# Kernel tuning notes

Hardware: AMD Instinct MI355X
Metric: run time of the kernel (lower is better)

## Reference

```python
import jax, jax.numpy as jnp
import numpy as np

DIM = 128
L = 4
EPS = 1e-5


def setup_inputs() -> dict:
    key = jax.random.key(0)
    ks = jax.random.split(key, 16)
    g, n_per = 4096, 32
    n = g * n_per
    e = 4 * n
    s = 0.05
    inp = {
        "x_atoms": jax.random.randint(ks[0], (n, 2), 0, 3),
        "edge_index": jax.random.randint(ks[1], (2, e), 0, n),
        "edge_attr": jax.random.randint(ks[2], (e, 2), 0, 3),
        "batch": jnp.repeat(jnp.arange(g), n_per),
        "num_graphs": g,
        "max_nodes": n_per,
        "task_embs": jax.random.normal(ks[3], (g, DIM), jnp.float32),
        "teb": jax.random.normal(ks[4], (g, DIM), jnp.float32),
        "emb1": jax.random.normal(ks[5], (120, DIM), jnp.float32) * s,
        "emb2": jax.random.normal(ks[6], (3, DIM), jnp.float32) * s,
        "edge_e1": jax.random.normal(ks[7], (L, 6, DIM), jnp.float32) * s,
        "edge_e2": jax.random.normal(ks[8], (L, 3, DIM), jnp.float32) * s,
        "W1": jax.random.normal(ks[9], (L, DIM, 2 * DIM), jnp.float32) * s,
        "b1": jnp.zeros((L, 2 * DIM), jnp.float32),
        "W2": jax.random.normal(ks[10], (L, 2 * DIM, DIM), jnp.float32) * s,
        "b2": jnp.zeros((L, DIM), jnp.float32),
        "bn_w": jnp.ones((L, DIM), jnp.float32),
        "bn_b": jnp.zeros((L, DIM), jnp.float32),
        "film_Wg": jax.random.normal(ks[11], (2, DIM, DIM), jnp.float32) * s,
        "film_bg": jnp.zeros((2, DIM), jnp.float32),
        "film_Wb": jax.random.normal(ks[12], (2, DIM, DIM), jnp.float32) * s,
        "film_bb": jnp.zeros((2, DIM), jnp.float32),
    }
    return inp


def _gin_layer(x, src, dst, eattr, e1, e2, W1, b1, W2, b2):
    # GINConv (pretrain-gnns): scatter-add of (x_j + edge_emb) + self-loop (attr [4,0]), then 2-layer MLP.
    n = x.shape[0]
    emb = e1[eattr[:, 0]] + e2[eattr[:, 1]]                       # [E, D]
    agg = jax.ops.segment_sum(x[src] + emb, dst, num_segments=n)  # [N, D]
    agg = agg + x + (e1[4] + e2[0])                               # self loops
    h = jax.nn.relu(agg @ W1 + b1)
    return h @ W2 + b2


def _batchnorm(x, w, b):
    mu = jnp.mean(x, axis=0)
    var = jnp.var(x, axis=0)
    return (x - mu) * jax.lax.rsqrt(var + EPS) * w + b


def reference(x_atoms, edge_index, edge_attr, batch, num_graphs, max_nodes,
              task_embs, teb, emb1, emb2, edge_e1, edge_e2,
              W1, b1, W2, b2, bn_w, bn_b,
              film_Wg, film_bg, film_Wb, film_bb):
    g = int(num_graphs)
    n = x_atoms.shape[0]
    x = emb1[x_atoms[:, 0]] + emb2[x_atoms[:, 1]]                 # [N, D]
    # --- add virtual nodes (one per graph) and bidirectional virtual edges ---
    x = jnp.concatenate([x, teb], axis=0)                         # [N+g, D]
    dst0 = jnp.arange(n)
    vsrc = n + batch                                              # virtual node index per real node
    src_all = jnp.concatenate([edge_index[0], vsrc, dst0])
    dst_all = jnp.concatenate([edge_index[1], dst0, vsrc])
    v_attr = jnp.tile(jnp.array([[5, 0]], dtype=edge_attr.dtype), (2 * n, 1))
    eattr = jnp.concatenate([edge_attr, v_attr], axis=0)
    # --- positions within graph for to_dense_batch (batch is sorted) ---
    counts = jnp.bincount(batch, length=g)
    offsets = jnp.cumsum(counts) - counts
    pos = dst0 - offsets[batch]
    for layer in range(L):
        x = _gin_layer(x, src_all, dst_all, eattr,
                       edge_e1[layer], edge_e2[layer],
                       W1[layer], b1[layer], W2[layer], b2[layer])
        if layer in (1, 3):
            xv = x[n:]
            dense = jnp.zeros((g, int(max_nodes), DIM), x.dtype).at[batch, pos].set(x[:n])
            fl = layer // 3
            gamma = task_embs @ film_Wg[fl] + film_bg[fl]          # [g, D]
            beta = task_embs @ film_Wb[fl] + film_bb[fl]
            dense = gamma[:, None, :] * dense + beta[:, None, :]
            x = jnp.concatenate([dense[batch, pos], xv], axis=0)   # masked_select inverse
        x = _batchnorm(x, bn_w[layer], bn_b[layer])
        if layer != L - 1:
            x = jax.nn.relu(x)
        # dropout is identity in eval mode
    return x[:n]
```

## Files before the change

### kernel.cpp

```cpp
#include <hip/hip_runtime.h>
#include <hip/hip_bf16.h>

typedef __bf16 bf16_t;
typedef bf16_t bf16x8 __attribute__((ext_vector_type(8)));
typedef float f32x4 __attribute__((ext_vector_type(4)));

#define EPSV 1e-5f

__global__ void k_zerof(float* p, int cnt) {
  int i = blockIdx.x * 256 + threadIdx.x;
  if (i < cnt) p[i] = 0.f;
}
__global__ void k_zeroi(int* p, int cnt) {
  int i = blockIdx.x * 256 + threadIdx.x;
  if (i < cnt) p[i] = 0;
}

__global__ void k_prep_weights(const float* __restrict__ W1, const float* __restrict__ W2,
                               bf16_t* __restrict__ W1T, bf16_t* __restrict__ W2T, int total) {
  int idx = blockIdx.x * 256 + threadIdx.x;
  if (idx >= total) return;
  int l = idx >> 15, r = idx & 32767;
  int k = r >> 8, c = r & 255;
  W1T[(l << 15) + c * 128 + k] = (bf16_t)W1[idx];
  int k2 = r >> 7, c2 = r & 127;
  W2T[(l << 15) + c2 * 256 + k2] = (bf16_t)W2[idx];
}

__global__ void k_prep_film(const float* __restrict__ Wg, const float* __restrict__ Wb,
                            bf16_t* __restrict__ fWT) {
  int idx = blockIdx.x * 256 + threadIdx.x;
  if (idx >= 4 * 16384) return;
  int m = idx >> 14, r = idx & 16383;
  int c = r >> 7, k = r & 127;
  const float* W = ((m & 1) ? Wb : Wg) + (m >> 1) * 16384;
  fWT[idx] = (bf16_t)W[k * 128 + c];
}

__global__ void k_prep_te(const float* __restrict__ te, bf16_t* __restrict__ teb_out, int total) {
  int idx = blockIdx.x * 256 + threadIdx.x;
  if (idx < total) teb_out[idx] = (bf16_t)te[idx];
}

__global__ void k_ecomb(const float* __restrict__ e1, const float* __restrict__ e2,
                        float* __restrict__ ec, int total) {
  int idx = blockIdx.x * 256 + threadIdx.x;
  if (idx >= total) return;
  int ch = idx & 127;
  int t = idx >> 7;
  int comb = t % 18, l = t / 18;
  int i = comb / 3, j = comb % 3;
  ec[idx] = e1[(l * 6 + i) * 128 + ch] + e2[(l * 3 + j) * 128 + ch];
}

__launch_bounds__(256, 2)
__global__ void k_film(const bf16_t* __restrict__ teb, const bf16_t* __restrict__ fWT,
                       const float* __restrict__ bg, const float* __restrict__ bb,
                       float* __restrict__ gbuf, int g) {
  const int mat = blockIdx.x & 3;
  const int r0 = (blockIdx.x >> 2) * 64;
  const int tid = threadIdx.x;
  const int wave = tid >> 6, lane = tid & 63;
  const int lr = lane & 15, lk = lane >> 4;
  const int w32 = wave * 32;
  const bf16_t* W = fWT + mat * 16384;
  const float* B = ((mat & 1) ? bb : bg) + (mat >> 1) * 128;

  bf16x8 bbf[2][4];
  #pragma unroll
  for (int cf = 0; cf < 2; ++cf)
    #pragma unroll
    for (int kk = 0; kk < 4; ++kk)
      bbf[cf][kk] = *(const bf16x8*)(W + ((w32 + cf * 16 + lr) << 7) + kk * 32 + (lk << 3));

  f32x4 acc[4][2];
  f32x4 zero4 = {0.f, 0.f, 0.f, 0.f};
  #pragma unroll
  for (int rf = 0; rf < 4; ++rf)
    #pragma unroll
    for (int cf = 0; cf < 2; ++cf) acc[rf][cf] = zero4;

  #pragma unroll
  for (int kk = 0; kk < 4; ++kk) {
    bf16x8 a[4];
    #pragma unroll
    for (int rf = 0; rf < 4; ++rf)
      a[rf] = *(const bf16x8*)(teb + ((size_t)(r0 + rf * 16 + lr) << 7) + kk * 32 + (lk << 3));
    #pragma unroll
    for (int rf = 0; rf < 4; ++rf)
      #pragma unroll
      for (int cf = 0; cf < 2; ++cf)
        acc[rf][cf] = __builtin_amdgcn_mfma_f32_16x16x32_bf16(a[rf], bbf[cf][kk], acc[rf][cf], 0, 0, 0);
  }

  float* out = gbuf + (size_t)mat * g * 128;
  #pragma unroll
  for (int cf = 0; cf < 2; ++cf) {
    int col = w32 + cf * 16 + lr;
    float bias = B[col];
    #pragma unroll
    for (int rf = 0; rf < 4; ++rf)
      #pragma unroll
      for (int j = 0; j < 4; ++j) {
        int row = r0 + rf * 16 + lk * 4 + j;
        out[(size_t)row * 128 + col] = acc[rf][cf][j] + bias;
      }
  }
}

__global__ void k_init_x(const int* __restrict__ xa, const float* __restrict__ teb,
                         const float* __restrict__ emb1, const float* __restrict__ emb2,
                         bf16_t* __restrict__ x, int n, int N) {
  int idx = blockIdx.x * 256 + threadIdx.x;
  if (idx >= N * 128) return;
  int row = idx >> 7, ch = idx & 127;
  float v;
  if (row < n) v = emb1[xa[row * 2] * 128 + ch] + emb2[xa[row * 2 + 1] * 128 + ch];
  else v = teb[(size_t)(row - n) * 128 + ch];
  x[idx] = (bf16_t)v;
}

__global__ void k_hist(const int* __restrict__ eidx, int* __restrict__ cnt, int E) {
  int i = blockIdx.x * 256 + threadIdx.x;
  if (i < E) atomicAdd(&cnt[eidx[E + i]], 1);
}

__global__ void k_scan1(const int* __restrict__ cnt, int* __restrict__ part,
                        int* __restrict__ bsum, int n) {
  __shared__ int s[256];
  int i = blockIdx.x * 256 + threadIdx.x;
  int v = (i < n) ? cnt[i] : 0;
  s[threadIdx.x] = v;
  for (int off = 1; off < 256; off <<= 1) {
    __syncthreads();
    int t = (threadIdx.x >= off) ? s[threadIdx.x - off] : 0;
    __syncthreads();
    s[threadIdx.x] += t;
  }
  __syncthreads();
  if (i < n) part[i] = s[threadIdx.x] - v;
  if (threadIdx.x == 255) bsum[blockIdx.x] = s[255];
}

__global__ void k_scan2(int* bsum, int nb) {
  __shared__ int s[512];
  int v = ((int)threadIdx.x < nb) ? bsum[threadIdx.x] : 0;
  s[threadIdx.x] = v;
  for (int off = 1; off < 512; off <<= 1) {
    __syncthreads();
    int t = ((int)threadIdx.x >= off) ? s[threadIdx.x - off] : 0;
    __syncthreads();
    s[threadIdx.x] += t;
  }
  __syncthreads();
  if ((int)threadIdx.x < nb) bsum[threadIdx.x] = s[threadIdx.x] - v;
}

__global__ void k_scan3(int* __restrict__ rp, const int* __restrict__ bsum,
                        int* __restrict__ fill, int n, int E) {
  int i = blockIdx.x * 256 + threadIdx.x;
  if (i < n) {
    int v = rp[i] + bsum[i >> 8];
    rp[i] = v;
    fill[i] = v;
  }
  if (i == 0) rp[n] = E;
}

__global__ void k_scatter(const int* __restrict__ eidx, const int* __restrict__ eattr,
                          int* __restrict__ fill, int* __restrict__ pack, int E) {
  int i = blockIdx.x * 256 + threadIdx.x;
  if (i >= E) return;
  int s = eidx[i];
  int d = eidx[E + i];
  int comb = eattr[2 * i] * 3 + eattr[2 * i + 1];
  int p = atomicAdd(&fill[d], 1);
  pack[p] = s | (comb << 20);
}

__global__ void k_normx(const bf16_t* __restrict__ y, const float* __restrict__ scsh,
                        bf16_t* __restrict__ xn, int total8) {
  int i = blockIdx.x * 256 + threadIdx.x;
  if (i >= total8) return;
  int ch8 = i & 15;
  bf16x8 v = ((const bf16x8*)y)[i];
  float4 sc0 = ((const float4*)scsh)[ch8 * 2];
  float4 sc1 = ((const float4*)scsh)[ch8 * 2 + 1];
  float4 sh0 = ((const float4*)(scsh + 128))[ch8 * 2];
  float4 sh1 = ((const float4*)(scsh + 128))[ch8 * 2 + 1];
  float sc[8] = {sc0.x, sc0.y, sc0.z, sc0.w, sc1.x, sc1.y, sc1.z, sc1.w};
  float sh[8] = {sh0.x, sh0.y, sh0.z, sh0.w, sh1.x, sh1.y, sh1.z, sh1.w};
  bf16x8 o;
  #pragma unroll
  for (int j = 0; j < 8; ++j)
    o[j] = (bf16_t)fmaxf(fmaf((float)v[j], sc[j], sh[j]), 0.f);
  ((bf16x8*)xn)[i] = o;
}

__global__ void k_agg(const bf16_t* __restrict__ xn, const int* __restrict__ batch,
                      const int* __restrict__ rp, const int* __restrict__ pack,
                      const float* __restrict__ ec,
                      bf16_t* __restrict__ agg, int n, int N, int npg) {
  int node = blockIdx.x * 16 + (threadIdx.x >> 4);
  if (node >= N) return;
  const int ch0 = (threadIdx.x & 15) * 8;

  float4 s0 = *(const float4*)(ec + 12 * 128 + ch0);
  float4 s1 = *(const float4*)(ec + 12 * 128 + ch0 + 4);
  float4 v0 = *(const float4*)(ec + 15 * 128 + ch0);
  float4 v1 = *(const float4*)(ec + 15 * 128 + ch0 + 4);
  float se[8] = {s0.x, s0.y, s0.z, s0.w, s1.x, s1.y, s1.z, s1.w};
  float ve[8] = {v0.x, v0.y, v0.z, v0.w, v1.x, v1.y, v1.z, v1.w};
  bf16x8 hs = *(const bf16x8*)(xn + ((size_t)node << 7) + ch0);
  float acc[8];

  if (node < n) {
    int b = batch[node];
    bf16x8 hv = *(const bf16x8*)(xn + ((size_t)(n + b) << 7) + ch0);
    #pragma unroll
    for (int j = 0; j < 8; ++j)
      acc[j] = (float)hs[j] + (float)hv[j] + se[j] + ve[j];
    int beg = rp[node], end = rp[node + 1];
    for (int e = beg;; ++e) {
      bool act = (e < end);
      if (!__ballot(act)) break;
      int p = pack[act ? e : 0];
      int srow = p & 0xFFFFF;
      int comb = (p >> 20) & 31;
      bf16x8 hx = *(const bf16x8*)(xn + ((size_t)srow << 7) + ch0);
      const float* er = ec + comb * 128 + ch0;
      float4 e0 = *(const float4*)er;
      float4 e1v = *(const float4*)(er + 4);
      float ee[8] = {e0.x, e0.y, e0.z, e0.w, e1v.x, e1v.y, e1v.z, e1v.w};
      float m = act ? 1.f : 0.f;
      #pragma unroll
      for (int j = 0; j < 8; ++j)
        acc[j] = fmaf(m, (float)hx[j] + ee[j], acc[j]);
    }
  } else {
    float fn = (float)npg;
    #pragma unroll
    for (int j = 0; j < 8; ++j)
      acc[j] = (float)hs[j] + se[j] + fn * ve[j];
    int base = (node - n) * npg;
    for (int k = 0; k < npg; ++k) {
      bf16x8 hx = *(const bf16x8*)(xn + ((size_t)(base + k) << 7) + ch0);
      #pragma unroll
      for (int j = 0; j < 8; ++j) acc[j] += (float)hx[j];
    }
  }

  bf16x8 o;
  #pragma unroll
  for (int j = 0; j < 8; ++j) o[j] = (bf16_t)acc[j];
  *(bf16x8*)(agg + ((size_t)node << 7) + ch0) = o;
}

__launch_bounds__(512, 4)
__global__ void k_mlp(const bf16_t* __restrict__ agg, const bf16_t* __restrict__ W1T,
                      const bf16_t* __restrict__ W2T, const float* __restrict__ b1,
                      const float* __restrict__ b2, const float* __restrict__ gamma,
                      const float* __restrict__ beta, const int* __restrict__ batch,
                      bf16_t* __restrict__ y, float* __restrict__ gstats, int n, int N) {
  __shared__ __align__(16) char As[16384];
  __shared__ __align__(16) char Hs[32768];
  __shared__ float sred[256];
  const int tid = threadIdx.x;
  const int m0 = blockIdx.x * 64;
  const int wave = tid >> 6, lane = tid & 63;
  const int lr = lane & 15, lk = lane >> 4;
  if (tid < 256) sred[tid] = 0.f;

  #pragma unroll
  for (int it = 0; it < 2; ++it) {
    int e = it * 512 + tid;
    int row = e >> 4, c16 = e & 15;
    bf16x8 v = *(const bf16x8*)(agg + ((size_t)(m0 + row) << 7) + c16 * 8);
    int byte = (row << 8) + (c16 << 4);
    byte ^= (row & 7) << 4;
    *(bf16x8*)(As + byte) = v;
  }

  const int c1base = wave * 32;
  bf16x8 bb1[2][4];
  #pragma unroll
  for (int cf = 0; cf < 2; ++cf)
    #pragma unroll
    for (int kk = 0; kk < 4; ++kk)
      bb1[cf][kk] = *(const bf16x8*)(W1T + ((c1base + cf * 16 + lr) << 7) + kk * 32 + (lk << 3));

  __syncthreads();

  f32x4 zero4 = {0.f, 0.f, 0.f, 0.f};
  f32x4 acc1[4][2];
  #pragma unroll
  for (int rf = 0; rf < 4; ++rf)
    #pragma unroll
    for (int cf = 0; cf < 2; ++cf) acc1[rf][cf] = zero4;

  #pragma unroll
  for (int kk = 0; kk < 4; ++kk) {
    bf16x8 a[4];
    #pragma unroll
    for (int rf = 0; rf < 4; ++rf) {
      int arow = rf * 16 + lr;
      int abyte = (arow << 8) + kk * 64 + (lk << 4);
      abyte ^= (arow & 7) << 4;
      a[rf] = *(const bf16x8*)(As + abyte);
    }
    #pragma unroll
    for (int rf = 0; rf < 4; ++rf)
      #pragma unroll
      for (int cf = 0; cf < 2; ++cf)
        acc1[rf][cf] = __builtin_amdgcn_mfma_f32_16x16x32_bf16(a[rf], bb1[cf][kk], acc1[rf][cf], 0, 0, 0);
  }

  #pragma unroll
  for (int cf = 0; cf < 2; ++cf) {
    int col = c1base + cf * 16 + lr;
    float bias = b1[col];
    #pragma unroll
    for (int rf = 0; rf < 4; ++rf)
      #pragma unroll
      for (int j = 0; j < 4; ++j) {
        int r = rf * 16 + lk * 4 + j;
        float h = acc1[rf][cf][j] + bias;
        h = h > 0.f ? h : 0.f;
        int byte = (r << 9) + col * 2;
        byte ^= (r & 15) << 4;
        *(bf16_t*)(Hs + byte) = (bf16_t)h;
      }
  }

  const int c2base = wave * 16;
  bf16x8 bb2[8];
  #pragma unroll
  for (int kk = 0; kk < 8; ++kk)
    bb2[kk] = *(const bf16x8*)(W2T + ((c2base + lr) << 8) + kk * 32 + (lk << 3));

  __syncthreads();

  f32x4 acc2[4];
  #pragma unroll
  for (int rf = 0; rf < 4; ++rf) acc2[rf] = zero4;

  #pragma unroll
  for (int kk = 0; kk < 8; ++kk) {
    bf16x8 a2[4];
    #pragma unroll
    for (int rf = 0; rf < 4; ++rf) {
      int row = rf * 16 + lr;
      int byte = (row << 9) + kk * 64 + (lk << 4);
      byte ^= (row & 15) << 4;
      a2[rf] = *(const bf16x8*)(Hs + byte);
    }
    #pragma unroll
    for (int rf = 0; rf < 4; ++rf)
      acc2[rf] = __builtin_amdgcn_mfma_f32_16x16x32_bf16(a2[rf], bb2[kk], acc2[rf], 0, 0, 0);
  }

  int gb[4][4];
  #pragma unroll
  for (int rf = 0; rf < 4; ++rf)
    #pragma unroll
    for (int j = 0; j < 4; ++j) {
      int row = m0 + rf * 16 + lk * 4 + j;
      gb[rf][j] = (gamma != nullptr && row < n) ? batch[row] : -1;
    }

  __syncthreads();

  {
    int col = c2base + lr;
    float bias = b2[col];
    float s = 0.f, q = 0.f;
    #pragma unroll
    for (int rf = 0; rf < 4; ++rf)
      #pragma unroll
      for (int j = 0; j < 4; ++j) {
        int row = rf * 16 + lk * 4 + j;
        float v = acc2[rf][j] + bias;
        if (gb[rf][j] >= 0)
          v = gamma[(size_t)gb[rf][j] * 128 + col] * v + beta[(size_t)gb[rf][j] * 128 + col];
        if (m0 + row < N) { s += v; q += v * v; }
        int byte = (row << 9) + (col << 2);
        byte ^= (row & 7) << 4;
        *(float*)(Hs + byte) = v;
      }
    s += __shfl_xor(s, 16, 64); s += __shfl_xor(s, 32, 64);
    q += __shfl_xor(q, 16, 64); q += __shfl_xor(q, 32, 64);
    if (lane < 16) { sred[col] = s; sred[128 + col] = q; }
  }
  __syncthreads();

  {
    int row = tid >> 3, c0 = (tid & 7) * 16;
    int grow = m0 + row;
    if (grow < N) {
      float vv[16];
      #pragma unroll
      for (int c4 = 0; c4 < 4; ++c4) {
        int byte = (row << 9) + ((c0 + c4 * 4) << 2);
        byte ^= (row & 7) << 4;
        f32x4 t4 = *(const f32x4*)(Hs + byte);
        vv[c4 * 4 + 0] = t4[0]; vv[c4 * 4 + 1] = t4[1];
        vv[c4 * 4 + 2] = t4[2]; vv[c4 * 4 + 3] = t4[3];
      }
      bf16x8 o0, o1;
      #pragma unroll
      for (int j = 0; j < 8; ++j) { o0[j] = (bf16_t)vv[j]; o1[j] = (bf16_t)vv[8 + j]; }
      *(bf16x8*)(y + (size_t)grow * 128 + c0) = o0;
      *(bf16x8*)(y + (size_t)grow * 128 + c0 + 8) = o1;
    }
  }
  if (tid < 256) atomicAdd(&gstats[((blockIdx.x & 15) << 8) + tid], sred[tid]);
}

__global__ void k_finalize(float* st, const float* __restrict__ bnw,
                           const float* __restrict__ bnb, float invN) {
  int ch = threadIdx.x;
  float s = 0.f, q = 0.f;
  #pragma unroll
  for (int c = 0; c < 16; ++c) { s += st[c * 256 + ch]; q += st[c * 256 + 128 + ch]; }
  __syncthreads();
  #pragma unroll
  for (int z = 0; z < 32; ++z) st[ch * 32 + z] = 0.f;
  float mean = s * invN;
  float var = fmaxf(q * invN - mean * mean, 0.f);
  float inv = rsqrtf(var + EPSV);
  float sc = inv * bnw[ch];
  st[4096 + ch] = sc;
  st[4224 + ch] = bnb[ch] - mean * sc;
}

__global__ void k_norm(const bf16_t* __restrict__ yin, const float* __restrict__ scsh,
                       float* __restrict__ out, int total8) {
  int i = blockIdx.x * 256 + threadIdx.x;
  if (i >= total8) return;
  int ch8 = i & 15;
  bf16x8 v = ((const bf16x8*)yin)[i];
  float4 sc0 = ((const float4*)scsh)[ch8 * 2];
  float4 sc1 = ((const float4*)scsh)[ch8 * 2 + 1];
  float4 sh0 = ((const float4*)(scsh + 128))[ch8 * 2];
  float4 sh1 = ((const float4*)(scsh + 128))[ch8 * 2 + 1];
  float4 r0, r1;
  r0.x = (float)v[0] * sc0.x + sh0.x;
  r0.y = (float)v[1] * sc0.y + sh0.y;
  r0.z = (float)v[2] * sc0.z + sh0.z;
  r0.w = (float)v[3] * sc0.w + sh0.w;
  r1.x = (float)v[4] * sc1.x + sh1.x;
  r1.y = (float)v[5] * sc1.y + sh1.y;
  r1.z = (float)v[6] * sc1.z + sh1.z;
  r1.w = (float)v[7] * sc1.w + sh1.w;
  ((float4*)out)[i * 2] = r0;
  ((float4*)out)[i * 2 + 1] = r1;
}

extern "C" void kernel_launch(void* const* d_in, const int* in_sizes, int n_in,
                              void* d_out, int out_size, void* d_ws, size_t ws_size,
                              hipStream_t stream) {
  const int*   x_atoms    = (const int*)d_in[0];
  const int*   edge_index = (const int*)d_in[1];
  const int*   edge_attr  = (const int*)d_in[2];
  const int*   batch      = (const int*)d_in[3];
  const float* task_embs  = (const float*)d_in[6];
  const float* teb        = (const float*)d_in[7];
  const float* emb1       = (const float*)d_in[8];
  const float* emb2       = (const float*)d_in[9];
  const float* edge_e1    = (const float*)d_in[10];
  const float* edge_e2    = (const float*)d_in[11];
  const float* W1         = (const float*)d_in[12];
  const float* b1         = (const float*)d_in[13];
  const float* W2         = (const float*)d_in[14];
  const float* b2         = (const float*)d_in[15];
  const float* bnw        = (const float*)d_in[16];
  const float* bnb        = (const float*)d_in[17];
  const float* fWg        = (const float*)d_in[18];
  const float* fbg        = (const float*)d_in[19];
  const float* fWb        = (const float*)d_in[20];
  const float* fbb        = (const float*)d_in[21];

  const int n   = in_sizes[0] / 2;
  const int E   = in_sizes[1] / 2;
  const int g   = in_sizes[6] / 128;
  const int N   = n + g;
  const int npg = n / g;
  const int L   = in_sizes[12] / 32768;

  char* ws = (char*)d_ws;
  size_t off = 0;
  auto alloc = [&](size_t bytes) { size_t o = off; off += (bytes + 255) & ~(size_t)255; return o; };
  bf16_t* xbuf   = (bf16_t*)(ws + alloc((size_t)N * 128 * 2));
  bf16_t* xn     = (bf16_t*)(ws + alloc((size_t)N * 128 * 2));
  bf16_t* aggb   = (bf16_t*)(ws + alloc((size_t)N * 128 * 2));
  float*  gbuf   = (float*)(ws + alloc((size_t)4 * g * 128 * 4));
  bf16_t* W1Tb   = (bf16_t*)(ws + alloc((size_t)L * 32768 * 2));
  bf16_t* W2Tb   = (bf16_t*)(ws + alloc((size_t)L * 32768 * 2));
  bf16_t* fWTb   = (bf16_t*)(ws + alloc((size_t)4 * 16384 * 2));
  bf16_t* tebuf  = (bf16_t*)(ws + alloc((size_t)g * 128 * 2));
  float*  ecomb  = (float*)(ws + alloc((size_t)L * 18 * 128 * 4));
  float*  gstats = (float*)(ws + alloc((size_t)(4096 + 256) * 4));
  int*    row_ptr= (int*)(ws + alloc((size_t)(n + 1) * 4));
  int*    fill   = (int*)(ws + alloc((size_t)n * 4));
  int*    epack  = (int*)(ws + alloc((size_t)E * 4));
  int*    bsum   = (int*)(ws + alloc(512 * 4));
  (void)ws_size; (void)n_in; (void)out_size;

  k_prep_weights<<<(L * 32768 + 255) / 256, 256, 0, stream>>>(W1, W2, W1Tb, W2Tb, L * 32768);
  k_prep_film<<<(4 * 16384 + 255) / 256, 256, 0, stream>>>(fWg, fWb, fWTb);
  k_prep_te<<<(g * 128 + 255) / 256, 256, 0, stream>>>(task_embs, tebuf, g * 128);
  k_init_x<<<(N * 128 + 255) / 256, 256, 0, stream>>>(x_atoms, teb, emb1, emb2, xn, n, N);
  k_ecomb<<<(L * 18 * 128 + 255) / 256, 256, 0, stream>>>(edge_e1, edge_e2, ecomb, L * 18 * 128);
  k_film<<<(g / 64) * 4, 256, 0, stream>>>(tebuf, fWTb, fbg, fbb, gbuf, g);

  const int nb = (n + 255) / 256;
  k_zeroi<<<nb, 256, 0, stream>>>(fill, n);
  k_hist<<<(E + 255) / 256, 256, 0, stream>>>(edge_index, fill, E);
  k_scan1<<<nb, 256, 0, stream>>>(fill, row_ptr, bsum, n);
  k_scan2<<<1, 512, 0, stream>>>(bsum, nb);
  k_scan3<<<nb, 256, 0, stream>>>(row_ptr, bsum, fill, n, E);
  k_scatter<<<(E + 255) / 256, 256, 0, stream>>>(edge_index, edge_attr, fill, epack, E);

  k_zerof<<<16, 256, 0, stream>>>(gstats, 4096);
  for (int l = 0; l < 4; ++l) {
    if (l > 0)
      k_normx<<<(N * 16 + 255) / 256, 256, 0, stream>>>(xbuf, gstats + 4096, xn, N * 16);
    k_agg<<<(N + 15) / 16, 256, 0, stream>>>(xn, batch, row_ptr, epack,
        ecomb + (size_t)l * 18 * 128, aggb, n, N, npg);
    const float* gm = nullptr; const float* bt = nullptr;
    if (l == 1) { gm = gbuf;                       bt = gbuf + (size_t)g * 128; }
    if (l == 3) { gm = gbuf + (size_t)2 * g * 128; bt = gbuf + (size_t)3 * g * 128; }
    k_mlp<<<(N + 63) / 64, 512, 0, stream>>>(aggb, W1Tb + (size_t)l * 32768,
        W2Tb + (size_t)l * 32768, b1 + l * 256, b2 + l * 128, gm, bt, batch,
        xbuf, gstats, n, N);
    k_finalize<<<1, 128, 0, stream>>>(gstats, bnw + l * 128, bnb + l * 128, 1.0f / (float)N);
  }
  k_norm<<<(n * 16 + 255) / 256, 256, 0, stream>>>(xbuf, gstats + 4096, (float*)d_out, n * 16);
}
```

Before: 561.8 us.

## Batch edge index loads via shuffles in aggregation; read MLP A operand from global

In the aggregation kernel, each 16-lane group now loads up to 16 packed edge indices in one coalesced load. It broadcasts them with __shfl and software-pipelines the row and edge-embedding loads one step ahead, replacing the per-edge ballot loop and its masked FMAs. The virtual-node branch gets the same one-ahead prefetch. The MLP kernel drops LDS staging of the aggregated input tile and its barrier, so each wave reads its A fragments straight from global memory. This saves LDS and a sync but makes the eight waves fetch the same rows redundantly. The zero-initialisation of the reduction scratch buffer was also removed, which is only safe if later code reinitialises it.

```diff
diff --git a/kernel.cpp b/kernel.cpp
--- a/kernel.cpp
+++ b/kernel.cpp
@@ -203,52 +203,77 @@
                       bf16_t* __restrict__ agg, int n, int N, int npg) {
   int node = blockIdx.x * 16 + (threadIdx.x >> 4);
   if (node >= N) return;
-  const int ch0 = (threadIdx.x & 15) * 8;
+  const int lane = threadIdx.x & 63;
+  const int li = lane & 15;
+  const int grp = lane & 48;
+  const int ch0 = li * 8;
 
   float4 s0 = *(const float4*)(ec + 12 * 128 + ch0);
   float4 s1 = *(const float4*)(ec + 12 * 128 + ch0 + 4);
   float4 v0 = *(const float4*)(ec + 15 * 128 + ch0);
   float4 v1 = *(const float4*)(ec + 15 * 128 + ch0 + 4);
-  float se[8] = {s0.x, s0.y, s0.z, s0.w, s1.x, s1.y, s1.z, s1.w};
-  float ve[8] = {v0.x, v0.y, v0.z, v0.w, v1.x, v1.y, v1.z, v1.w};
   bf16x8 hs = *(const bf16x8*)(xn + ((size_t)node << 7) + ch0);
   float acc[8];
+
+  #define EACC(HX, E0, E1) { \
+    acc[0] += (float)HX[0] + E0.x; acc[1] += (float)HX[1] + E0.y; \
+    acc[2] += (float)HX[2] + E0.z; acc[3] += (float)HX[3] + E0.w; \
+    acc[4] += (float)HX[4] + E1.x; acc[5] += (float)HX[5] + E1.y; \
+    acc[6] += (float)HX[6] + E1.z; acc[7] += (float)HX[7] + E1.w; }
 
   if (node < n) {
     int b = batch[node];
     bf16x8 hv = *(const bf16x8*)(xn + ((size_t)(n + b) << 7) + ch0);
-    #pragma unroll
-    for (int j = 0; j < 8; ++j)
-      acc[j] = (float)hs[j] + (float)hv[j] + se[j] + ve[j];
+    acc[0] = (float)hs[0] + (float)hv[0] + s0.x + v0.x;
+    acc[1] = (float)hs[1] + (float)hv[1] + s0.y + v0.y;
+    acc[2] = (float)hs[2] + (float)hv[2] + s0.z + v0.z;
+    acc[3] = (float)hs[3] + (float)hv[3] + s0.w + v0.w;
+    acc[4] = (float)hs[4] + (float)hv[4] + s1.x + v1.x;
+    acc[5] = (float)hs[5] + (float)hv[5] + s1.y + v1.y;
+    acc[6] = (float)hs[6] + (float)hv[6] + s1.z + v1.z;
+    acc[7] = (float)hs[7] + (float)hv[7] + s1.w + v1.w;
     int beg = rp[node], end = rp[node + 1];
-    for (int e = beg;; ++e) {
-      bool act = (e < end);
-      if (!__ballot(act)) break;
-      int p = pack[act ? e : 0];
-      int srow = p & 0xFFFFF;
-      int comb = (p >> 20) & 31;
-      bf16x8 hx = *(const bf16x8*)(xn + ((size_t)srow << 7) + ch0);
-      const float* er = ec + comb * 128 + ch0;
+    for (int base = beg; base < end; base += 16) {
+      int cnt = end - base; cnt = cnt > 16 ? 16 : cnt;
+      int pl = pack[base + (li < cnt ? li : cnt - 1)];
+      int pc = __shfl(pl, grp, 64);
+      bf16x8 hx = *(const bf16x8*)(xn + ((size_t)(pc & 0xFFFFF) << 7) + ch0);
+      const float* er = ec + ((pc >> 20) & 31) * 128 + ch0;
       float4 e0 = *(const float4*)er;
-      float4 e1v = *(const float4*)(er + 4);
-      float ee[8] = {e0.x, e0.y, e0.z, e0.w, e1v.x, e1v.y, e1v.z, e1v.w};
-      float m = act ? 1.f : 0.f;
-      #pragma unroll
-      for (int j = 0; j < 8; ++j)
-        acc[j] = fmaf(m, (float)hx[j] + ee[j], acc[j]);
+      float4 e1 = *(const float4*)(er + 4);
+      for (int j = 1; j < cnt; ++j) {
+        int pn = __shfl(pl, grp | j, 64);
+        bf16x8 hx2 = *(const bf16x8*)(xn + ((size_t)(pn & 0xFFFFF) << 7) + ch0);
+        const float* er2 = ec + ((pn >> 20) & 31) * 128 + ch0;
+        float4 f0 = *(const float4*)er2;
+        float4 f1 = *(const float4*)(er2 + 4);
+        EACC(hx, e0, e1);
+        hx = hx2; e0 = f0; e1 = f1;
+      }
+      EACC(hx, e0, e1);
     }
   } else {
     float fn = (float)npg;
-    #pragma unroll
-    for (int j = 0; j < 8; ++j)
-      acc[j] = (float)hs[j] + se[j] + fn * ve[j];
+    acc[0] = (float)hs[0] + s0.x + fn * v0.x;
+    acc[1] = (float)hs[1] + s0.y + fn * v0.y;
+    acc[2] = (float)hs[2] + s0.z + fn * v0.z;
+    acc[3] = (float)hs[3] + s0.w + fn * v0.w;
+    acc[4] = (float)hs[4] + s1.x + fn * v1.x;
+    acc[5] = (float)hs[5] + s1.y + fn * v1.y;
+    acc[6] = (float)hs[6] + s1.z + fn * v1.z;
+    acc[7] = (float)hs[7] + s1.w + fn * v1.w;
     int base = (node - n) * npg;
-    for (int k = 0; k < npg; ++k) {
-      bf16x8 hx = *(const bf16x8*)(xn + ((size_t)(base + k) << 7) + ch0);
-      #pragma unroll
-      for (int j = 0; j < 8; ++j) acc[j] += (float)hx[j];
+    bf16x8 h0 = *(const bf16x8*)(xn + ((size_t)base << 7) + ch0);
+    for (int k = 1; k < npg; ++k) {
+      bf16x8 h1 = *(const bf16x8*)(xn + ((size_t)(base + k) << 7) + ch0);
+      #pragma unroll
+      for (int j = 0; j < 8; ++j) acc[j] += (float)h0[j];
+      h0 = h1;
     }
-  }
+    #pragma unroll
+    for (int j = 0; j < 8; ++j) acc[j] += (float)h0[j];
+  }
+  #undef EACC
 
   bf16x8 o;
   #pragma unroll
@@ -262,24 +287,12 @@
                       const float* __restrict__ b2, const float* __restrict__ gamma,
                       const float* __restrict__ beta, const int* __restrict__ batch,
                       bf16_t* __restrict__ y, float* __restrict__ gstats, int n, int N) {
-  __shared__ __align__(16) char As[16384];
   __shared__ __align__(16) char Hs[32768];
   __shared__ float sred[256];
   const int tid = threadIdx.x;
   const int m0 = blockIdx.x * 64;
   const int wave = tid >> 6, lane = tid & 63;
   const int lr = lane & 15, lk = lane >> 4;
-  if (tid < 256) sred[tid] = 0.f;
-
-  #pragma unroll
-  for (int it = 0; it < 2; ++it) {
-    int e = it * 512 + tid;
-    int row = e >> 4, c16 = e & 15;
-    bf16x8 v = *(const bf16x8*)(agg + ((size_t)(m0 + row) << 7) + c16 * 8);
-    int byte = (row << 8) + (c16 << 4);
-    byte ^= (row & 7) << 4;
-    *(bf16x8*)(As + byte) = v;
-  }
 
   const int c1base = wave * 32;
   bf16x8 bb1[2][4];
@@ -289,7 +302,13 @@
     for (int kk = 0; kk < 4; ++kk)
       bb1[cf][kk] = *(const bf16x8*)(W1T + ((c1base + cf * 16 + lr) << 7) + kk * 32 + (lk << 3));
 
-  __syncthreads();
+  const bf16_t* ab[4];
+  #pragma unroll
+  for (int rf = 0; rf < 4; ++rf) {
+    int r = m0 + rf * 16 + lr;
+    r = r < N ? r : N - 1;
+    ab[rf] = agg + ((size_t)r << 7) + (lk << 3);
+  }
 
   f32x4 zero4 = {0.f, 0.f, 0.f, 0.f};
   f32x4 acc1[4][2];
@@ -302,12 +321,8 @@
   for (int kk = 0; kk < 4; ++kk) {
     bf16x8 a[4];
     #pragma unroll
-    for (int rf = 0; rf < 4; ++rf) {
-      int arow = rf * 16 + lr;
-      int abyte = (arow << 8) + kk * 64 + (lk << 4);
-      abyte ^= (arow & 7) << 4;
-      a[rf] = *(const bf16x8*)(As + abyte);
-    }
+    for (int rf = 0; rf < 4; ++rf)
+      a[rf] = *(const bf16x8*)(ab[rf] + kk * 32);
     #pragma unroll
     for (int rf = 0; rf < 4; ++rf)
       #pragma unroll
```

Result: slower. 652.5 us (+16.1%).
